# Optimization experiments

Hardware: AMD Instinct MI355X
Metric: run time of the kernel (lower is better)

Reference implementation:

```python
import math
import jax, jax.numpy as jnp
import numpy as np

THETA = 10000.0

def _rotate_half(x):
    # lucidrains interleaved pairs: (d r) with r=2
    x = x.reshape(*x.shape[:-1], -1, 2)
    x1, x2 = x[..., 0], x[..., 1]
    return jnp.stack([-x2, x1], axis=-1).reshape(*x.shape[:-2], -1)

def _apply_rotary(x):
    # x: [B, H, S, D]
    seq_len, d = x.shape[-2], x.shape[-1]
    inv_freq = 1.0 / (THETA ** (jnp.arange(0, d, 2, dtype=jnp.float32) / d))  # [D/2]
    t = jnp.arange(seq_len, dtype=jnp.float32)
    freqs = t[:, None] * inv_freq[None, :]                 # [S, D/2]
    freqs = jnp.repeat(freqs, 2, axis=-1)                  # [S, D] interleaved
    cos, sin = jnp.cos(freqs), jnp.sin(freqs)
    return x * cos + _rotate_half(x) * sin

def setup_inputs() -> dict:
    key = jax.random.key(0)
    k1, k2, k3, k4 = jax.random.split(key, 4)
    B, H, S, D = 2, 16, 2048, 64
    q = jax.random.normal(k1, (B, H, S, D), dtype=jnp.float32)
    k = jax.random.normal(k2, (B, H, S, D), dtype=jnp.float32)
    v = jax.random.normal(k3, (B, H, S, D), dtype=jnp.float32)
    mask = jax.random.randint(k4, (B, 1, S, S), 0, 2, dtype=jnp.int32)
    return {"q": q, "k": k, "v": v, "mask": mask}

def reference(q, k, v, mask):
    d = k.shape[-1]
    qr = _apply_rotary(q)
    kr = _apply_rotary(k)
    score = jnp.einsum('bhqd,bhkd->bhqk', qr, kr) / math.sqrt(d)
    score = jnp.where(mask == 0, jnp.float32(-10000.0), score)
    score = jax.nn.softmax(score, axis=-1)
    out = jnp.einsum('bhqk,bhkd->bhqd', score, v)
    return (out, score)
```

## Files before the change

kernel.cpp:

```cpp
#include <hip/hip_runtime.h>
#include <hip/hip_fp16.h>

#define NB 2
#define NH 16
#define NS 2048
#define ND 64

typedef __attribute__((ext_vector_type(8))) _Float16 half8;
typedef __attribute__((ext_vector_type(4))) _Float16 half4;
typedef __attribute__((ext_vector_type(4))) float float4v;

static constexpr int NE = NB * NH * NS * ND;
static constexpr int TPB = 512;

__device__ __forceinline__ void wg_barrier_lds() {
    asm volatile("s_waitcnt lgkmcnt(0)" ::: "memory");
    __builtin_amdgcn_s_barrier();
    __builtin_amdgcn_sched_barrier(0);
}

static constexpr int ROPE_BLKS = (NE / 2) / 256;
static constexpr int VT_BLKS   = NE / 256;
static constexpr int MP_BLKS   = (NB * NS * NS) / 256;

__global__ void prep_kernel(const float* __restrict__ q,
                            const float* __restrict__ k,
                            const float* __restrict__ v,
                            const int* __restrict__ mask,
                            _Float16* __restrict__ qr,
                            _Float16* __restrict__ kr6,
                            _Float16* __restrict__ v4,
                            unsigned int* __restrict__ mp) {
    int blk = blockIdx.x;
    if (blk < ROPE_BLKS) {
        int idx = blk * 256 + threadIdx.x;
        int i   = idx & 31;
        int row = idx >> 5;
        int s   = row & (NS - 1);
        int bh  = row >> 11;

        float inv_freq = expf((float)i * -0.2878231366242710f);
        float ang = (float)s * inv_freq;
        float sn, cs;
        sincosf(ang, &sn, &cs);

        size_t base = (size_t)row * ND + 2 * i;
        float q0 = q[base], q1 = q[base + 1];
        float k0 = k[base], k1 = k[base + 1];
        qr[base]     = (_Float16)(q0 * cs - q1 * sn);
        qr[base + 1] = (_Float16)(q1 * cs + q0 * sn);

        int oct = i >> 2;
        int j0  = (2 * i) & 7;
        size_t t6 = ((size_t)(bh * 128 + (s >> 4)) * 8 + oct) * 128 + (s & 15) * 8 + j0;
        kr6[t6]     = (_Float16)(k0 * cs - k1 * sn);
        kr6[t6 + 1] = (_Float16)(k1 * cs + k0 * sn);
    } else if (blk < ROPE_BLKS + VT_BLKS) {
        int idx = (blk - ROPE_BLKS) * 256 + threadIdx.x;
        int j    = idx & 3;
        int lm   = (idx >> 2) & 15;
        int kq   = (idx >> 6) & 3;
        int dblk = (idx >> 8) & 3;
        int kt   = (idx >> 10) & 127;
        int bh   = idx >> 17;
        int key  = kt * 16 + kq * 4 + j;
        int d    = dblk * 16 + lm;
        v4[idx] = (_Float16)v[((size_t)bh * NS + key) * ND + d];
    } else {
        size_t idx = (size_t)(blk - ROPE_BLKS - VT_BLKS) * 256 + threadIdx.x;
        unsigned long long bal = __ballot(mask[idx] != 0);
        int l = threadIdx.x & 63;
        if (l == 0)       mp[idx >> 5] = (unsigned int)bal;
        else if (l == 32) mp[idx >> 5] = (unsigned int)(bal >> 32);
    }
}

__global__ __launch_bounds__(TPB, 4)
void attn_reg_kernel(const _Float16* __restrict__ qr,
                     const _Float16* __restrict__ kr6,
                     const _Float16* __restrict__ v4,
                     const unsigned int* __restrict__ mp,
                     float* __restrict__ out,
                     float* __restrict__ score) {
    __shared__ unsigned int maskb[16 * 64];
    __shared__ float        sums8[8][16];
    __shared__ float        outb[8 * 16 * 64];

    int wgid = (blockIdx.x & 7) * 512 + (blockIdx.x >> 3);
    int qt = wgid & 127;
    int bh = wgid >> 7;
    int b  = bh >> 4;
    int q0 = qt * 16;

    int tid = threadIdx.x;
    int w   = tid >> 6;
    int l   = tid & 63;
    int lm  = l & 15;
    int lp  = l >> 4;

    {
        const unsigned int* mrow = mp + ((size_t)b * NS + q0) * 64;
        for (int i = tid; i < 16 * 64; i += TPB) maskb[i] = mrow[i];
    }

    const _Float16* qrow = qr + ((size_t)bh * NS + q0 + lm) * ND;
    half8 a0 = *(const half8*)(qrow + lp * 8);
    half8 a1 = *(const half8*)(qrow + 32 + lp * 8);
    const _Float16* k6 = kr6 + (size_t)bh * 128 * 1024;
    wg_barrier_lds();

    half4 earr[16];
    float ps = 0.0f;
#pragma unroll
    for (int t = 0; t < 16; ++t) {
        int kt = w * 16 + t;
        const _Float16* kp = k6 + (size_t)kt * 1024 + l * 8;
        half8 b0 = *(const half8*)(kp);
        half8 b1 = *(const half8*)(kp + 512);
        float4v acc = {0.f, 0.f, 0.f, 0.f};
        acc = __builtin_amdgcn_mfma_f32_16x16x32_f16(b0, a0, acc, 0, 0, 0);
        acc = __builtin_amdgcn_mfma_f32_16x16x32_f16(b1, a1, acc, 0, 0, 0);
        int keyb = kt * 16 + lp * 4;
        unsigned int mw = maskb[lm * 64 + (keyb >> 5)];
        int bit0 = keyb & 31;
        half4 ep;
#pragma unroll
        for (int r = 0; r < 4; ++r) {
            float ev = ((mw >> (bit0 + r)) & 1u) ? __expf(acc[r] * 0.125f) : 0.0f;
            ps += ev;
            ep[r] = (_Float16)ev;
        }
        earr[t] = ep;
    }
    ps += __shfl_xor(ps, 16);
    ps += __shfl_xor(ps, 32);
    if (lp == 0) sums8[w][lm] = ps;
    wg_barrier_lds();

    {
        float s = 0.0f;
#pragma unroll
        for (int ww = 0; ww < 8; ++ww) s += sums8[ww][lm];
        float iv = (s > 0.0f) ? (1.0f / s) : 0.0f;
        float* srow = score + ((size_t)bh * NS + q0 + lm) * NS + w * 256 + lp * 4;

        float4v ac0 = {0.f, 0.f, 0.f, 0.f};
        float4v ac1 = {0.f, 0.f, 0.f, 0.f};
        float4v ac2 = {0.f, 0.f, 0.f, 0.f};
        float4v ac3 = {0.f, 0.f, 0.f, 0.f};
        const _Float16* vb = v4 + (size_t)bh * 128 * 1024 + l * 4;
#pragma unroll
        for (int st = 0; st < 16; ++st) {
            half4 e = earr[st];
            float4v f;
            f[0] = (float)e[0] * iv;
            f[1] = (float)e[1] * iv;
            f[2] = (float)e[2] * iv;
            f[3] = (float)e[3] * iv;
            __builtin_nontemporal_store(f, (float4v*)(srow + st * 16));

            int kt = w * 16 + st;
            const _Float16* vp = vb + (size_t)kt * 1024;
            half4 af0 = *(const half4*)(vp);
            half4 af1 = *(const half4*)(vp + 256);
            half4 af2 = *(const half4*)(vp + 512);
            half4 af3 = *(const half4*)(vp + 768);
            __builtin_amdgcn_s_setprio(1);
            ac0 = __builtin_amdgcn_mfma_f32_16x16x16f16(af0, e, ac0, 0, 0, 0);
            ac1 = __builtin_amdgcn_mfma_f32_16x16x16f16(af1, e, ac1, 0, 0, 0);
            ac2 = __builtin_amdgcn_mfma_f32_16x16x16f16(af2, e, ac2, 0, 0, 0);
            ac3 = __builtin_amdgcn_mfma_f32_16x16x16f16(af3, e, ac3, 0, 0, 0);
            __builtin_amdgcn_s_setprio(0);
        }
        float* ow = outb + w * 1024 + lm * 64 + lp * 4;
#pragma unroll
        for (int r = 0; r < 4; ++r) {
            ow[ 0 + r] = ac0[r];
            ow[16 + r] = ac1[r];
            ow[32 + r] = ac2[r];
            ow[48 + r] = ac3[r];
        }
    }
    wg_barrier_lds();

    {
        float* orow = out + ((size_t)bh * NS + q0) * ND;
        for (int i = tid; i < 16 * 64; i += TPB) {
            int r = i >> 6;
            float s = 0.0f;
#pragma unroll
            for (int ww = 0; ww < 8; ++ww) s += sums8[ww][r];
            float iv = (s > 0.0f) ? (1.0f / s) : 0.0f;
            float acc = 0.0f;
#pragma unroll
            for (int ww = 0; ww < 8; ++ww) acc += outb[ww * 1024 + i];
            __builtin_nontemporal_store(acc * iv, &orow[i]);
        }
    }
}

extern "C" void kernel_launch(void* const* d_in, const int* in_sizes, int n_in,
                              void* d_out, int out_size, void* d_ws, size_t ws_size,
                              hipStream_t stream) {
    const float* q    = (const float*)d_in[0];
    const float* k    = (const float*)d_in[1];
    const float* v    = (const float*)d_in[2];
    const int*   mask = (const int*)d_in[3];

    float* out   = (float*)d_out;
    float* score = out + (size_t)NE;

    _Float16* qrw = (_Float16*)d_ws;
    _Float16* kr6 = qrw + NE;
    _Float16* v4w = kr6 + NE;
    unsigned int* mp = (unsigned int*)(v4w + NE);

    prep_kernel<<<dim3(ROPE_BLKS + VT_BLKS + MP_BLKS), dim3(256), 0, stream>>>(
        q, k, v, mask, qrw, kr6, v4w, mp);
    attn_reg_kernel<<<dim3(NB * NH * (NS / 16)), dim3(TPB), 0, stream>>>(
        qrw, kr6, v4w, mp, out, score);
}
```

Baseline: 208.9 us.

## Precompute softmax row sums in separate pass, stream scores without buffering

Adds a sums_kernel that computes QK^T, masked exp and the per-row inverse sum ahead of time. The main kernel can then normalize and store each score tile immediately and feed it to the PV MFMA in the same loop. This removes the intra-workgroup barrier between the exp pass and the output pass, and drops the 16-entry earr register array. In exchange the QK^T and exp work is done twice, plus an extra launch and more global reads of K and the mask.

```diff
diff --git a/kernel.cpp b/kernel.cpp
--- a/kernel.cpp
+++ b/kernel.cpp
@@ -75,15 +75,61 @@
     }
 }
 
+__global__ __launch_bounds__(256, 8)
+void sums_kernel(const _Float16* __restrict__ qr,
+                 const _Float16* __restrict__ kr6,
+                 const unsigned int* __restrict__ mp,
+                 float* __restrict__ ginvs) {
+    int wgid = (blockIdx.x & 7) * 128 + (blockIdx.x >> 3);
+    int qt4 = wgid & 31;
+    int bh  = wgid >> 5;
+    int b   = bh >> 4;
+
+    int tid = threadIdx.x;
+    int w   = tid >> 6;
+    int l   = tid & 63;
+    int lm  = l & 15;
+    int lp  = l >> 4;
+    int q0  = (qt4 * 4 + w) * 16;
+
+    const _Float16* qrow = qr + ((size_t)bh * NS + q0 + lm) * ND;
+    half8 a0 = *(const half8*)(qrow + lp * 8);
+    half8 a1 = *(const half8*)(qrow + 32 + lp * 8);
+    const _Float16* k6 = kr6 + (size_t)bh * 128 * 1024;
+    const unsigned int* mrow = mp + ((size_t)b * NS + q0) * 64;
+
+    float ps = 0.0f;
+#pragma unroll 8
+    for (int kt = 0; kt < 128; ++kt) {
+        const _Float16* kp = k6 + (size_t)kt * 1024 + l * 8;
+        half8 b0 = *(const half8*)(kp);
+        half8 b1 = *(const half8*)(kp + 512);
+        float4v acc = {0.f, 0.f, 0.f, 0.f};
+        acc = __builtin_amdgcn_mfma_f32_16x16x32_f16(b0, a0, acc, 0, 0, 0);
+        acc = __builtin_amdgcn_mfma_f32_16x16x32_f16(b1, a1, acc, 0, 0, 0);
+        int keyb = kt * 16 + lp * 4;
+        unsigned int mw = mrow[(size_t)lm * 64 + (keyb >> 5)];
+        int bit0 = keyb & 31;
+#pragma unroll
+        for (int r = 0; r < 4; ++r)
+            ps += ((mw >> (bit0 + r)) & 1u) ? __expf(acc[r] * 0.125f) : 0.0f;
+    }
+    ps += __shfl_xor(ps, 16);
+    ps += __shfl_xor(ps, 32);
+    if (lp == 0)
+        ginvs[(size_t)bh * NS + q0 + lm] = (ps > 0.0f) ? (1.0f / ps) : 0.0f;
+}
+
 __global__ __launch_bounds__(TPB, 4)
-void attn_reg_kernel(const _Float16* __restrict__ qr,
-                     const _Float16* __restrict__ kr6,
-                     const _Float16* __restrict__ v4,
-                     const unsigned int* __restrict__ mp,
-                     float* __restrict__ out,
-                     float* __restrict__ score) {
+void attn_stream_kernel(const _Float16* __restrict__ qr,
+                        const _Float16* __restrict__ kr6,
+                        const _Float16* __restrict__ v4,
+                        const unsigned int* __restrict__ mp,
+                        const float* __restrict__ ginvs,
+                        float* __restrict__ out,
+                        float* __restrict__ score) {
     __shared__ unsigned int maskb[16 * 64];
-    __shared__ float        sums8[8][16];
+    __shared__ float        ivs[16];
     __shared__ float        outb[8 * 16 * 64];
 
     int wgid = (blockIdx.x & 7) * 512 + (blockIdx.x >> 3);
@@ -102,15 +148,21 @@
         const unsigned int* mrow = mp + ((size_t)b * NS + q0) * 64;
         for (int i = tid; i < 16 * 64; i += TPB) maskb[i] = mrow[i];
     }
-
+    float iv = ginvs[(size_t)bh * NS + q0 + lm];
+    if (w == 0 && lp == 0) ivs[lm] = iv;
     const _Float16* qrow = qr + ((size_t)bh * NS + q0 + lm) * ND;
     half8 a0 = *(const half8*)(qrow + lp * 8);
     half8 a1 = *(const half8*)(qrow + 32 + lp * 8);
     const _Float16* k6 = kr6 + (size_t)bh * 128 * 1024;
     wg_barrier_lds();
 
-    half4 earr[16];
-    float ps = 0.0f;
+    float4v ac0 = {0.f, 0.f, 0.f, 0.f};
+    float4v ac1 = {0.f, 0.f, 0.f, 0.f};
+    float4v ac2 = {0.f, 0.f, 0.f, 0.f};
+    float4v ac3 = {0.f, 0.f, 0.f, 0.f};
+    const _Float16* vb = v4 + (size_t)bh * 128 * 1024 + l * 4;
+    float* srow = score + ((size_t)bh * NS + q0 + lm) * NS + w * 256 + lp * 4;
+
 #pragma unroll
     for (int t = 0; t < 16; ++t) {
         int kt = w * 16 + t;
@@ -123,55 +175,32 @@
         int keyb = kt * 16 + lp * 4;
         unsigned int mw = maskb[lm * 64 + (keyb >> 5)];
         int bit0 = keyb & 31;
+        float e0 = ((mw >> (bit0 + 0)) & 1u) ? __expf(acc[0] * 0.125f) : 0.0f;
+        float e1 = ((mw >> (bit0 + 1)) & 1u) ? __expf(acc[1] * 0.125f) : 0.0f;
+        float e2 = ((mw >> (bit0 + 2)) & 1u) ? __expf(acc[2] * 0.125f) : 0.0f;
+        float e3 = ((mw >> (bit0 + 3)) & 1u) ? __expf(acc[3] * 0.125f) : 0.0f;
+
+        float4v f;
+        f[0] = e0 * iv; f[1] = e1 * iv; f[2] = e2 * iv; f[3] = e3 * iv;
+        __builtin_nontemporal_store(f, (float4v*)(srow + t * 16));
+
         half4 ep;
-#pragma unroll
-        for (int r = 0; r < 4; ++r) {
-            float ev = ((mw >> (bit0 + r)) & 1u) ? __expf(acc[r] * 0.125f) : 0.0f;
-            ps += ev;
-            ep[r] = (_Float16)ev;
-        }
-        earr[t] = ep;
-    }
-    ps += __shfl_xor(ps, 16);
-    ps += __shfl_xor(ps, 32);
-    if (lp == 0) sums8[w][lm] = ps;
-    wg_barrier_lds();
+        ep[0] = (_Float16)e0; ep[1] = (_Float16)e1;
+        ep[2] = (_Float16)e2; ep[3] = (_Float16)e3;
+        const _Float16* vp = vb + (size_t)kt * 1024;
+        half4 af0 = *(const half4*)(vp);
+        half4 af1 = *(const half4*)(vp + 256);
+        half4 af2 = *(const half4*)(vp + 512);
+        half4 af3 = *(const half4*)(vp + 768);
+        __builtin_amdgcn_s_setprio(1);
+        ac0 = __builtin_amdgcn_mfma_f32_16x16x16f16(af0, ep, ac0, 0, 0, 0);
+        ac1 = __builtin_amdgcn_mfma_f32_16x16x16f16(af1, ep, ac1, 0, 0, 0);
+        ac2 = __builtin_amdgcn_mfma_f32_16x16x16f16(af2, ep, ac2, 0, 0, 0);
+        ac3 = __builtin_amdgcn_mfma_f32_16x16x16f16(af3, ep, ac3, 0, 0, 0);
+        __builtin_amdgcn_s_setprio(0);
+    }
 
     {
-        float s = 0.0f;
-#pragma unroll
-        for (int ww = 0; ww < 8; ++ww) s += sums8[ww][lm];
-        float iv = (s > 0.0f) ? (1.0f / s) : 0.0f;
-        float* srow = score + ((size_t)bh * NS + q0 + lm) * NS + w * 256 + lp * 4;
-
-        float4v ac0 = {0.f, 0.f, 0.f, 0.f};
-        float4v ac1 = {0.f, 0.f, 0.f, 0.f};
-        float4v ac2 = {0.f, 0.f, 0.f, 0.f};
-        float4v ac3 = {0.f, 0.f, 0.f, 0.f};
-        const _Float16* vb = v4 + (size_t)bh * 128 * 1024 + l * 4;
-#pragma unroll
-        for (int st = 0; st < 16; ++st) {
-            half4 e = earr[st];
-            float4v f;
-            f[0] = (float)e[0] * iv;
-            f[1] = (float)e[1] * iv;
-            f[2] = (float)e[2] * iv;
-            f[3] = (float)e[3] * iv;
-            __builtin_nontemporal_store(f, (float4v*)(srow + st * 16));
-
-            int kt = w * 16 + st;
-            const _Float16* vp = vb + (size_t)kt * 1024;
-            half4 af0 = *(const half4*)(vp);
-            half4 af1 = *(const half4*)(vp + 256);
-            half4 af2 = *(const half4*)(vp + 512);
-            half4 af3 = *(const half4*)(vp + 768);
-            __builtin_amdgcn_s_setprio(1);
-            ac0 = __builtin_amdgcn_mfma_f32_16x16x16f16(af0, e, ac0, 0, 0, 0);
-            ac1 = __builtin_amdgcn_mfma_f32_16x16x16f16(af1, e, ac1, 0, 0, 0);
-            ac2 = __builtin_amdgcn_mfma_f32_16x16x16f16(af2, e, ac2, 0, 0, 0);
-            ac3 = __builtin_amdgcn_mfma_f32_16x16x16f16(af3, e, ac3, 0, 0, 0);
-            __builtin_amdgcn_s_setprio(0);
-        }
         float* ow = outb + w * 1024 + lm * 64 + lp * 4;
 #pragma unroll
         for (int r = 0; r < 4; ++r) {
@@ -187,14 +216,10 @@
         float* orow = out + ((size_t)bh * NS + q0) * ND;
         for (int i = tid; i < 16 * 64; i += TPB) {
             int r = i >> 6;
-            float s = 0.0f;
-#pragma unroll
-            for (int ww = 0; ww < 8; ++ww) s += sums8[ww][r];
-            float iv = (s > 0.0f) ? (1.0f / s) : 0.0f;
             float acc = 0.0f;
 #pragma unroll
             for (int ww = 0; ww < 8; ++ww) acc += outb[ww * 1024 + i];
-            __builtin_nontemporal_store(acc * iv, &orow[i]);
+            __builtin_nontemporal_store(acc * ivs[r], &orow[i]);
         }
     }
 }
@@ -214,9 +239,12 @@
     _Float16* kr6 = qrw + NE;
     _Float16* v4w = kr6 + NE;
     unsigned int* mp = (unsigned int*)(v4w + NE);
+    float* ginvs = (float*)(mp + (size_t)NB * NS * NS / 32);
 
     prep_kernel<<<dim3(ROPE_BLKS + VT_BLKS + MP_BLKS), dim3(256), 0, stream>>>(
         q, k, v, mask, qrw, kr6, v4w, mp);
-    attn_reg_kernel<<<dim3(NB * NH * (NS / 16)), dim3(TPB), 0, stream>>>(
-        qrw, kr6, v4w, mp, out, score);
-}
+    sums_kernel<<<dim3(NB * NH * (NS / 64)), dim3(256), 0, stream>>>(
+        qrw, kr6, mp, ginvs);
+    attn_stream_kernel<<<dim3(NB * NH * (NS / 16)), dim3(TPB), 0, stream>>>(
+        qrw, kr6, v4w, mp, ginvs, out, score);
+}
```

After: 253.0 us. 1.21x slower.

## Fuse PV MFMA into score loop and stage probabilities in LDS for row-contiguous stores

Applied to the files above, without the earlier changes.

The P·V MFMAs move into the QK loop, consuming unnormalized fp16 probabilities right away, so the 16-entry register array of probabilities is no longer needed. The probabilities are written into a padded per-wave LDS slice, then read back transposed so each wave stores full contiguous 1KB row segments of the score matrix, not scattered 16-byte chunks. The LDS slice is reused for the output partial-sum reduction. This trades extra LDS traffic and a wait for better-coalesced global stores of the large score tensor and lower register pressure.

```diff
diff --git a/kernel.cpp b/kernel.cpp
--- a/kernel.cpp
+++ b/kernel.cpp
@@ -75,6 +75,9 @@
     }
 }
 
+static constexpr int TPH    = 264;
+static constexpr int WSLICE = 16 * TPH;
+
 __global__ __launch_bounds__(TPB, 4)
 void attn_reg_kernel(const _Float16* __restrict__ qr,
                      const _Float16* __restrict__ kr6,
@@ -84,7 +87,7 @@
                      float* __restrict__ score) {
     __shared__ unsigned int maskb[16 * 64];
     __shared__ float        sums8[8][16];
-    __shared__ float        outb[8 * 16 * 64];
+    __shared__ _Float16     pool[8 * WSLICE];
 
     int wgid = (blockIdx.x & 7) * 512 + (blockIdx.x >> 3);
     int qt = wgid & 127;
@@ -107,9 +110,14 @@
     half8 a0 = *(const half8*)(qrow + lp * 8);
     half8 a1 = *(const half8*)(qrow + 32 + lp * 8);
     const _Float16* k6 = kr6 + (size_t)bh * 128 * 1024;
+    _Float16* tw = pool + w * WSLICE;
     wg_barrier_lds();
 
-    half4 earr[16];
+    float4v ac0 = {0.f, 0.f, 0.f, 0.f};
+    float4v ac1 = {0.f, 0.f, 0.f, 0.f};
+    float4v ac2 = {0.f, 0.f, 0.f, 0.f};
+    float4v ac3 = {0.f, 0.f, 0.f, 0.f};
+    const _Float16* vb = v4 + (size_t)bh * 128 * 1024 + l * 4;
     float ps = 0.0f;
 #pragma unroll
     for (int t = 0; t < 16; ++t) {
@@ -130,7 +138,19 @@
             ps += ev;
             ep[r] = (_Float16)ev;
         }
-        earr[t] = ep;
+        *(half4*)(tw + lm * TPH + t * 16 + lp * 4) = ep;
+
+        const _Float16* vp = vb + (size_t)kt * 1024;
+        half4 af0 = *(const half4*)(vp);
+        half4 af1 = *(const half4*)(vp + 256);
+        half4 af2 = *(const half4*)(vp + 512);
+        half4 af3 = *(const half4*)(vp + 768);
+        __builtin_amdgcn_s_setprio(1);
+        ac0 = __builtin_amdgcn_mfma_f32_16x16x16f16(af0, ep, ac0, 0, 0, 0);
+        ac1 = __builtin_amdgcn_mfma_f32_16x16x16f16(af1, ep, ac1, 0, 0, 0);
+        ac2 = __builtin_amdgcn_mfma_f32_16x16x16f16(af2, ep, ac2, 0, 0, 0);
+        ac3 = __builtin_amdgcn_mfma_f32_16x16x16f16(af3, ep, ac3, 0, 0, 0);
+        __builtin_amdgcn_s_setprio(0);
     }
     ps += __shfl_xor(ps, 16);
     ps += __shfl_xor(ps, 32);
@@ -142,37 +162,24 @@
 #pragma unroll
         for (int ww = 0; ww < 8; ++ww) s += sums8[ww][lm];
         float iv = (s > 0.0f) ? (1.0f / s) : 0.0f;
-        float* srow = score + ((size_t)bh * NS + q0 + lm) * NS + w * 256 + lp * 4;
-
-        float4v ac0 = {0.f, 0.f, 0.f, 0.f};
-        float4v ac1 = {0.f, 0.f, 0.f, 0.f};
-        float4v ac2 = {0.f, 0.f, 0.f, 0.f};
-        float4v ac3 = {0.f, 0.f, 0.f, 0.f};
-        const _Float16* vb = v4 + (size_t)bh * 128 * 1024 + l * 4;
-#pragma unroll
-        for (int st = 0; st < 16; ++st) {
-            half4 e = earr[st];
+        float* sbase = score + ((size_t)bh * NS + q0) * NS + w * 256;
+#pragma unroll
+        for (int r = 0; r < 16; ++r) {
+            float ivr = __shfl(iv, r);
+            half4 hv = *(const half4*)(tw + r * TPH + l * 4);
             float4v f;
-            f[0] = (float)e[0] * iv;
-            f[1] = (float)e[1] * iv;
-            f[2] = (float)e[2] * iv;
-            f[3] = (float)e[3] * iv;
-            __builtin_nontemporal_store(f, (float4v*)(srow + st * 16));
-
-            int kt = w * 16 + st;
-            const _Float16* vp = vb + (size_t)kt * 1024;
-            half4 af0 = *(const half4*)(vp);
-            half4 af1 = *(const half4*)(vp + 256);
-            half4 af2 = *(const half4*)(vp + 512);
-            half4 af3 = *(const half4*)(vp + 768);
-            __builtin_amdgcn_s_setprio(1);
-            ac0 = __builtin_amdgcn_mfma_f32_16x16x16f16(af0, e, ac0, 0, 0, 0);
-            ac1 = __builtin_amdgcn_mfma_f32_16x16x16f16(af1, e, ac1, 0, 0, 0);
-            ac2 = __builtin_amdgcn_mfma_f32_16x16x16f16(af2, e, ac2, 0, 0, 0);
-            ac3 = __builtin_amdgcn_mfma_f32_16x16x16f16(af3, e, ac3, 0, 0, 0);
-            __builtin_amdgcn_s_setprio(0);
-        }
-        float* ow = outb + w * 1024 + lm * 64 + lp * 4;
+            f[0] = (float)hv[0] * ivr;
+            f[1] = (float)hv[1] * ivr;
+            f[2] = (float)hv[2] * ivr;
+            f[3] = (float)hv[3] * ivr;
+            __builtin_nontemporal_store(f, (float4v*)(sbase + (size_t)r * NS + l * 4));
+        }
+    }
+    asm volatile("s_waitcnt lgkmcnt(0)" ::: "memory");
+    __builtin_amdgcn_sched_barrier(0);
+
+    {
+        float* ow = (float*)tw + lm * 64 + lp * 4;
 #pragma unroll
         for (int r = 0; r < 4; ++r) {
             ow[ 0 + r] = ac0[r];
@@ -193,7 +200,8 @@
             float iv = (s > 0.0f) ? (1.0f / s) : 0.0f;
             float acc = 0.0f;
 #pragma unroll
-            for (int ww = 0; ww < 8; ++ww) acc += outb[ww * 1024 + i];
+            for (int ww = 0; ww < 8; ++ww)
+                acc += ((const float*)(pool + ww * WSLICE))[i];
             __builtin_nontemporal_store(acc * iv, &orow[i]);
         }
     }
```

After: 171.3 us (median of 2 runs). 18.0% less time.

## Pipeline attention across eight query tiles per workgroup with LDS double buffering

Applied to the files above, without the earlier changes.

Each workgroup now processes eight consecutive 16-row query tiles instead of one. It computes QK, exp and PV in a single pass, staging unnormalized probabilities in a double-buffered LDS transpose area. The normalized score rows of the previous tile are written out coalesced while the current tile computes, and the next tile's mask is prefetched. This aims to overlap the large score-store traffic with MFMA work and to make score writes row-contiguous. The cost is more LDS use, occupancy lowered to 2 waves per SIMD, and fewer workgroups (512).

```diff
diff --git a/kernel.cpp b/kernel.cpp
--- a/kernel.cpp
+++ b/kernel.cpp
@@ -10,7 +10,7 @@
 typedef __attribute__((ext_vector_type(4))) _Float16 half4;
 typedef __attribute__((ext_vector_type(4))) float float4v;
 
-static constexpr int NE = NB * NH * NS * ND;
+static constexpr int NE  = NB * NH * NS * ND;
 static constexpr int TPB = 512;
 
 __device__ __forceinline__ void wg_barrier_lds() {
@@ -75,22 +75,126 @@
     }
 }
 
-__global__ __launch_bounds__(TPB, 4)
-void attn_reg_kernel(const _Float16* __restrict__ qr,
-                     const _Float16* __restrict__ kr6,
-                     const _Float16* __restrict__ v4,
-                     const unsigned int* __restrict__ mp,
-                     float* __restrict__ out,
-                     float* __restrict__ score) {
-    __shared__ unsigned int maskb[16 * 64];
-    __shared__ float        sums8[8][16];
-    __shared__ float        outb[8 * 16 * 64];
-
-    int wgid = (blockIdx.x & 7) * 512 + (blockIdx.x >> 3);
-    int qt = wgid & 127;
-    int bh = wgid >> 7;
-    int b  = bh >> 4;
-    int q0 = qt * 16;
+static constexpr int TPH     = 264;
+static constexpr int WSLICE  = 16 * TPH;
+static constexpr int T_TILES = 8;
+static constexpr int TRANS_B = 2 * 8 * WSLICE * 2;
+static constexpr int MASK_OFF = TRANS_B;
+static constexpr int SUMS_OFF = TRANS_B + 8192;
+static constexpr int LDS_BYTES = SUMS_OFF + 1024;
+
+#define TILE_BODY(I, CUR, PREV, DOPREV, DOPREF)                                 \
+  do {                                                                          \
+    const int i_   = (I);                                                       \
+    const int cb_  = i_ & 1, pb_ = cb_ ^ 1;                                     \
+    const int q0c_ = q00 + i_ * 16;                                             \
+    const int q0p_ = q00 + (i_ - 1) * 16;                                       \
+    _Float16* twc = trans + (size_t)(cb_ * 8 + w) * WSLICE;                     \
+    _Float16* twp = trans + (size_t)(pb_ * 8 + w) * WSLICE;                     \
+    const _Float16* qrow = qr + ((size_t)bh * NS + q0c_ + lm) * ND;             \
+    half8 a0 = *(const half8*)(qrow + lp * 8);                                  \
+    half8 a1 = *(const half8*)(qrow + 32 + lp * 8);                             \
+    _Pragma("unroll") for (int r = 0; r < 4; ++r)                               \
+        CUR[r] = (float4v){0.f, 0.f, 0.f, 0.f};                                 \
+    float ivp = 0.0f;                                                           \
+    if (DOPREV) {                                                               \
+      float s_ = 0.0f;                                                          \
+      _Pragma("unroll") for (int ww = 0; ww < 8; ++ww)                          \
+          s_ += sums8[pb_ * 128 + ww * 16 + lm];                                \
+      ivp = (s_ > 0.0f) ? (1.0f / s_) : 0.0f;                                   \
+    }                                                                           \
+    float* sprev = score + ((size_t)bh * NS + q0p_) * NS + w * 256;             \
+    float ps = 0.0f;                                                            \
+    _Pragma("unroll 4")                                                         \
+    for (int t = 0; t < 16; ++t) {                                              \
+      int kt = w * 16 + t;                                                      \
+      const _Float16* kp = k6 + (size_t)kt * 1024 + l * 8;                      \
+      half8 b0 = *(const half8*)(kp);                                           \
+      half8 b1 = *(const half8*)(kp + 512);                                     \
+      const _Float16* vp = vb + (size_t)kt * 1024;                              \
+      half4 af0 = *(const half4*)(vp);                                          \
+      half4 af1 = *(const half4*)(vp + 256);                                    \
+      half4 af2 = *(const half4*)(vp + 512);                                    \
+      half4 af3 = *(const half4*)(vp + 768);                                    \
+      float4v acc = {0.f, 0.f, 0.f, 0.f};                                       \
+      acc = __builtin_amdgcn_mfma_f32_16x16x32_f16(b0, a0, acc, 0, 0, 0);       \
+      acc = __builtin_amdgcn_mfma_f32_16x16x32_f16(b1, a1, acc, 0, 0, 0);       \
+      int keyb = kt * 16 + lp * 4;                                              \
+      unsigned int mw = maskb[cb_ * 1024 + lm * 64 + (keyb >> 5)];              \
+      int bit0 = keyb & 31;                                                     \
+      half4 ep;                                                                 \
+      _Pragma("unroll") for (int r = 0; r < 4; ++r) {                           \
+        float ev = ((mw >> (bit0 + r)) & 1u) ? __expf(acc[r] * 0.125f) : 0.0f;  \
+        ps += ev;                                                               \
+        ep[r] = (_Float16)ev;                                                   \
+      }                                                                         \
+      *(half4*)(twc + lm * TPH + t * 16 + lp * 4) = ep;                         \
+      __builtin_amdgcn_s_setprio(1);                                            \
+      CUR[0] = __builtin_amdgcn_mfma_f32_16x16x16f16(af0, ep, CUR[0], 0, 0, 0); \
+      CUR[1] = __builtin_amdgcn_mfma_f32_16x16x16f16(af1, ep, CUR[1], 0, 0, 0); \
+      CUR[2] = __builtin_amdgcn_mfma_f32_16x16x16f16(af2, ep, CUR[2], 0, 0, 0); \
+      CUR[3] = __builtin_amdgcn_mfma_f32_16x16x16f16(af3, ep, CUR[3], 0, 0, 0); \
+      __builtin_amdgcn_s_setprio(0);                                            \
+      if (DOPREV) {              \
+        float ivr = __shfl(ivp, t);                                             \
+        half4 hv = *(const half4*)(twp + t * TPH + l * 4);                      \
+        float4v f_;                                                             \
+        f_[0] = (float)hv[0] * ivr; f_[1] = (float)hv[1] * ivr;                 \
+        f_[2] = (float)hv[2] * ivr; f_[3] = (float)hv[3] * ivr;                 \
+        __builtin_nontemporal_store(f_, (float4v*)(sprev + (size_t)t * NS + l * 4)); \
+      }                                                                         \
+    }                                                                           \
+    if (DOPREF) {          \
+      const unsigned int* mnext = mp + ((size_t)b * NS + q00 + (i_ + 1) * 16) * 64; \
+      for (int j = tid; j < 1024; j += TPB) maskb[pb_ * 1024 + j] = mnext[j];   \
+    }                                                                           \
+    ps += __shfl_xor(ps, 16);                                                   \
+    ps += __shfl_xor(ps, 32);                                                   \
+    if (lp == 0) sums8[cb_ * 128 + w * 16 + lm] = ps;                           \
+    if (DOPREV) {      \
+      asm volatile("s_waitcnt lgkmcnt(0)" ::: "memory");                        \
+      __builtin_amdgcn_sched_barrier(0);                                        \
+      float* ow = (float*)twp + lm * 64 + lp * 4;                               \
+      _Pragma("unroll") for (int r = 0; r < 4; ++r) {                           \
+        ow[ 0 + r] = PREV[0][r]; ow[16 + r] = PREV[1][r];                       \
+        ow[32 + r] = PREV[2][r]; ow[48 + r] = PREV[3][r];                       \
+      }                                                                         \
+    }                                                                           \
+    wg_barrier_lds();                                                           \
+    if (DOPREV) {            \
+      float* orow = out + ((size_t)bh * NS + q0p_) * ND;                        \
+      for (int j = tid; j < 1024; j += TPB) {                                   \
+        int r_ = j >> 6;                                                        \
+        float s_ = 0.0f;                                                        \
+        _Pragma("unroll") for (int ww = 0; ww < 8; ++ww)                        \
+            s_ += sums8[pb_ * 128 + ww * 16 + r_];                              \
+        float iv_ = (s_ > 0.0f) ? (1.0f / s_) : 0.0f;                           \
+        float a_ = 0.0f;                                                        \
+        _Pragma("unroll") for (int ww = 0; ww < 8; ++ww)                        \
+            a_ += ((const float*)(trans + (size_t)(pb_ * 8 + ww) * WSLICE))[j]; \
+        __builtin_nontemporal_store(a_ * iv_, &orow[j]);                        \
+      }                                                                         \
+      wg_barrier_lds();     \
+    }                                                                           \
+  } while (0)
+
+__global__ __launch_bounds__(TPB, 2)
+void attn_pipe_kernel(const _Float16* __restrict__ qr,
+                      const _Float16* __restrict__ kr6,
+                      const _Float16* __restrict__ v4,
+                      const unsigned int* __restrict__ mp,
+                      float* __restrict__ out,
+                      float* __restrict__ score) {
+    extern __shared__ char lds_raw[];
+    _Float16*     trans = (_Float16*)lds_raw;
+    unsigned int* maskb = (unsigned int*)(lds_raw + MASK_OFF);
+    float*        sums8 = (float*)(lds_raw + SUMS_OFF);
+
+    int wgid = (blockIdx.x & 7) * 64 + (blockIdx.x >> 3);
+    int g0  = wgid * T_TILES;
+    int bh  = g0 >> 7;
+    int b   = bh >> 4;
+    int q00 = (g0 & 127) * 16;
 
     int tid = threadIdx.x;
     int w   = tid >> 6;
@@ -98,103 +202,63 @@
     int lm  = l & 15;
     int lp  = l >> 4;
 
+    const _Float16* k6 = kr6 + (size_t)bh * 128 * 1024;
+    const _Float16* vb = v4 + (size_t)bh * 128 * 1024 + l * 4;
+
     {
-        const unsigned int* mrow = mp + ((size_t)b * NS + q0) * 64;
-        for (int i = tid; i < 16 * 64; i += TPB) maskb[i] = mrow[i];
-    }
-
-    const _Float16* qrow = qr + ((size_t)bh * NS + q0 + lm) * ND;
-    half8 a0 = *(const half8*)(qrow + lp * 8);
-    half8 a1 = *(const half8*)(qrow + 32 + lp * 8);
-    const _Float16* k6 = kr6 + (size_t)bh * 128 * 1024;
+        const unsigned int* m0 = mp + ((size_t)b * NS + q00) * 64;
+        for (int j = tid; j < 1024; j += TPB) maskb[j] = m0[j];
+    }
     wg_barrier_lds();
 
-    half4 earr[16];
-    float ps = 0.0f;
-#pragma unroll
-    for (int t = 0; t < 16; ++t) {
-        int kt = w * 16 + t;
-        const _Float16* kp = k6 + (size_t)kt * 1024 + l * 8;
-        half8 b0 = *(const half8*)(kp);
-        half8 b1 = *(const half8*)(kp + 512);
-        float4v acc = {0.f, 0.f, 0.f, 0.f};
-        acc = __builtin_amdgcn_mfma_f32_16x16x32_f16(b0, a0, acc, 0, 0, 0);
-        acc = __builtin_amdgcn_mfma_f32_16x16x32_f16(b1, a1, acc, 0, 0, 0);
-        int keyb = kt * 16 + lp * 4;
-        unsigned int mw = maskb[lm * 64 + (keyb >> 5)];
-        int bit0 = keyb & 31;
-        half4 ep;
+    float4v accA[4], accB[4];
+    TILE_BODY(0, accA, accB, false, true);
+#pragma unroll 1
+    for (int i = 1; i <= 5; i += 2) {
+        TILE_BODY(i,     accB, accA, true, true);
+        TILE_BODY(i + 1, accA, accB, true, true);
+    }
+    TILE_BODY(7, accB, accA, true, false);
+
+    {
+        const int pb_ = 1;
+        const int q0p_ = q00 + 7 * 16;
+        _Float16* twp = trans + (size_t)(pb_ * 8 + w) * WSLICE;
+        float s_ = 0.0f;
+#pragma unroll
+        for (int ww = 0; ww < 8; ++ww) s_ += sums8[pb_ * 128 + ww * 16 + lm];
+        float ivp = (s_ > 0.0f) ? (1.0f / s_) : 0.0f;
+        float* sprev = score + ((size_t)bh * NS + q0p_) * NS + w * 256;
+#pragma unroll 4
+        for (int t = 0; t < 16; ++t) {
+            float ivr = __shfl(ivp, t);
+            half4 hv = *(const half4*)(twp + t * TPH + l * 4);
+            float4v f_;
+            f_[0] = (float)hv[0] * ivr; f_[1] = (float)hv[1] * ivr;
+            f_[2] = (float)hv[2] * ivr; f_[3] = (float)hv[3] * ivr;
+            __builtin_nontemporal_store(f_, (float4v*)(sprev + (size_t)t * NS + l * 4));
+        }
+        asm volatile("s_waitcnt lgkmcnt(0)" ::: "memory");
+        __builtin_amdgcn_sched_barrier(0);
+        float* ow = (float*)twp + lm * 64 + lp * 4;
 #pragma unroll
         for (int r = 0; r < 4; ++r) {
-            float ev = ((mw >> (bit0 + r)) & 1u) ? __expf(acc[r] * 0.125f) : 0.0f;
-            ps += ev;
-            ep[r] = (_Float16)ev;
+            ow[ 0 + r] = accB[0][r]; ow[16 + r] = accB[1][r];
+            ow[32 + r] = accB[2][r]; ow[48 + r] = accB[3][r];
         }
-        earr[t] = ep;
-    }
-    ps += __shfl_xor(ps, 16);
-    ps += __shfl_xor(ps, 32);
-    if (lp == 0) sums8[w][lm] = ps;
-    wg_barrier_lds();
-
-    {
-        float s = 0.0f;
-#pragma unroll
-        for (int ww = 0; ww < 8; ++ww) s += sums8[ww][lm];
-        float iv = (s > 0.0f) ? (1.0f / s) : 0.0f;
-        float* srow = score + ((size_t)bh * NS + q0 + lm) * NS + w * 256 + lp * 4;
-
-        float4v ac0 = {0.f, 0.f, 0.f, 0.f};
-        float4v ac1 = {0.f, 0.f, 0.f, 0.f};
-        float4v ac2 = {0.f, 0.f, 0.f, 0.f};
-        float4v ac3 = {0.f, 0.f, 0.f, 0.f};
-        const _Float16* vb = v4 + (size_t)bh * 128 * 1024 + l * 4;
-#pragma unroll
-        for (int st = 0; st < 16; ++st) {
-            half4 e = earr[st];
-            float4v f;
-            f[0] = (float)e[0] * iv;
-            f[1] = (float)e[1] * iv;
-            f[2] = (float)e[2] * iv;
-            f[3] = (float)e[3] * iv;
-            __builtin_nontemporal_store(f, (float4v*)(srow + st * 16));
-
-            int kt = w * 16 + st;
-            const _Float16* vp = vb + (size_t)kt * 1024;
-            half4 af0 = *(const half4*)(vp);
-            half4 af1 = *(const half4*)(vp + 256);
-            half4 af2 = *(const half4*)(vp + 512);
-            half4 af3 = *(const half4*)(vp + 768);
-            __builtin_amdgcn_s_setprio(1);
-            ac0 = __builtin_amdgcn_mfma_f32_16x16x16f16(af0, e, ac0, 0, 0, 0);
-            ac1 = __builtin_amdgcn_mfma_f32_16x16x16f16(af1, e, ac1, 0, 0, 0);
-            ac2 = __builtin_amdgcn_mfma_f32_16x16x16f16(af2, e, ac2, 0, 0, 0);
-            ac3 = __builtin_amdgcn_mfma_f32_16x16x16f16(af3, e, ac3, 0, 0, 0);
-            __builtin_amdgcn_s_setprio(0);
-        }
-        float* ow = outb + w * 1024 + lm * 64 + lp * 4;
-#pragma unroll
-        for (int r = 0; r < 4; ++r) {
-            ow[ 0 + r] = ac0[r];
-            ow[16 + r] = ac1[r];
-            ow[32 + r] = ac2[r];
-            ow[48 + r] = ac3[r];
-        }
-    }
-    wg_barrier_lds();
-
-    {
-        float* orow = out + ((size_t)bh * NS + q0) * ND;
-        for (int i = tid; i < 16 * 64; i += TPB) {
-            int r = i >> 6;
-            float s = 0.0f;
-#pragma unroll
-            for (int ww = 0; ww < 8; ++ww) s += sums8[ww][r];
-            float iv = (s > 0.0f) ? (1.0f / s) : 0.0f;
-            float acc = 0.0f;
-#pragma unroll
-            for (int ww = 0; ww < 8; ++ww) acc += outb[ww * 1024 + i];
-            __builtin_nontemporal_store(acc * iv, &orow[i]);
+        wg_barrier_lds();
+        float* orow = out + ((size_t)bh * NS + q0p_) * ND;
+        for (int j = tid; j < 1024; j += TPB) {
+            int r_ = j >> 6;
+            float ss = 0.0f;
+#pragma unroll
+            for (int ww = 0; ww < 8; ++ww) ss += sums8[pb_ * 128 + ww * 16 + r_];
+            float iv_ = (ss > 0.0f) ? (1.0f / ss) : 0.0f;
+            float a_ = 0.0f;
+#pragma unroll
+            for (int ww = 0; ww < 8; ++ww)
+                a_ += ((const float*)(trans + (size_t)(pb_ * 8 + ww) * WSLICE))[j];
+            __builtin_nontemporal_store(a_ * iv_, &orow[j]);
         }
     }
 }
@@ -215,8 +279,12 @@
     _Float16* v4w = kr6 + NE;
     unsigned int* mp = (unsigned int*)(v4w + NE);
 
+    static_assert(LDS_BYTES <= 160 * 1024, "LDS budget");
+    (void)hipFuncSetAttribute(reinterpret_cast<const void*>(&attn_pipe_kernel),
+                              hipFuncAttributeMaxDynamicSharedMemorySize, LDS_BYTES);
+
     prep_kernel<<<dim3(ROPE_BLKS + VT_BLKS + MP_BLKS), dim3(256), 0, stream>>>(
         q, k, v, mask, qrw, kr6, v4w, mp);
-    attn_reg_kernel<<<dim3(NB * NH * (NS / 16)), dim3(TPB), 0, stream>>>(
+    attn_pipe_kernel<<<dim3(NB * NH * (NS / 16) / T_TILES), dim3(TPB), LDS_BYTES, stream>>>(
         qrw, kr6, v4w, mp, out, score);
 }
```

Result: faster. 201.2 us (-3.7%).
